# Performance work log

Measured on AMD Instinct MI355X. Metric: run time of the kernel, lower is better.

## Reference

```python
import jax, jax.numpy as jnp
import numpy as np

B, N, C = 4, 1029, 1024
H = 16           # num_heads
L = 8            # num_blocks
DH = C // H      # head_dim = 64
HID = 4 * C      # mlp hidden
SCALE = DH ** -0.5
EPS = 1e-6


def _ln(x, w, b):
    mu = jnp.mean(x, axis=-1, keepdims=True)
    var = jnp.var(x, axis=-1, keepdims=True)
    return (x - mu) * jax.lax.rsqrt(var + EPS) * w + b


def setup_inputs() -> dict:
    key = jax.random.key(0)
    ks = jax.random.split(key, 16)
    s = 0.02
    return {
        "x": jax.random.normal(ks[0], (B, N, C), dtype=jnp.float32),
        "ln1_w": jnp.ones((L, C), jnp.float32),
        "ln1_b": jnp.zeros((L, C), jnp.float32),
        "qkv_w": jax.random.normal(ks[1], (L, 3 * C, C), jnp.float32) * s,
        "qkv_b": jnp.zeros((L, 3 * C), jnp.float32),
        "proj_w": jax.random.normal(ks[2], (L, C, C), jnp.float32) * s,
        "proj_b": jnp.zeros((L, C), jnp.float32),
        "ln2_w": jnp.ones((L, C), jnp.float32),
        "ln2_b": jnp.zeros((L, C), jnp.float32),
        "fc1_w": jax.random.normal(ks[3], (L, HID, C), jnp.float32) * s,
        "fc1_b": jnp.zeros((L, HID), jnp.float32),
        "fc2_w": jax.random.normal(ks[4], (L, C, HID), jnp.float32) * s,
        "fc2_b": jnp.zeros((L, C), jnp.float32),
        "norm_w": jnp.ones((C,), jnp.float32),
        "norm_b": jnp.zeros((C,), jnp.float32),
    }


def _block(x, p):
    ln1_w, ln1_b, qkv_w, qkv_b, proj_w, proj_b, ln2_w, ln2_b, fc1_w, fc1_b, fc2_w, fc2_b = p
    # --- attention (manual fp32 QK^T / softmax / AV, as in Attention.forward) ---
    h = _ln(x, ln1_w, ln1_b)
    qkv = h @ qkv_w.T + qkv_b                        # [B,N,3C]
    qkv = qkv.reshape(B, N, 3, H, DH).transpose(2, 0, 3, 1, 4)  # [3,B,H,N,DH]
    q, k, v = qkv[0], qkv[1], qkv[2]
    attn = jnp.einsum("bhnd,bhmd->bhnm", q.astype(jnp.float32), k.astype(jnp.float32)) * SCALE
    # original subtracts row max before softmax; jax.nn.softmax is the same stable math
    attn = jax.nn.softmax(attn, axis=-1).astype(v.dtype)
    o = jnp.einsum("bhnm,bhmd->bhnd", attn, v)       # [B,H,N,DH]
    o = o.transpose(0, 2, 1, 3).reshape(B, N, C)
    x = x + (o @ proj_w.T + proj_b)
    # --- MLP (exact GELU, as nn.GELU default) ---
    h = _ln(x, ln2_w, ln2_b)
    h = jax.nn.gelu(h @ fc1_w.T + fc1_b, approximate=False)
    x = x + (h @ fc2_w.T + fc2_b)
    return x


def reference(x, ln1_w, ln1_b, qkv_w, qkv_b, proj_w, proj_b, ln2_w, ln2_b,
              fc1_w, fc1_b, fc2_w, fc2_b, norm_w, norm_b):
    params = (ln1_w, ln1_b, qkv_w, qkv_b, proj_w, proj_b, ln2_w, ln2_b,
              fc1_w, fc1_b, fc2_w, fc2_b)

    def body(h, p):
        return _block(h, p), None

    x, _ = jax.lax.scan(body, x, params)
    return _ln(x, norm_w, norm_b)
```

## Files before the change

kernel.cpp:

```cpp
#include <hip/hip_runtime.h>
#include <cstdint>
#include <cstddef>

#define B_    4
#define N_TOK 1029
#define C_    1024
#define H_    16
#define L_    8
#define HID_  4096
#define M_TOK (B_*N_TOK)
#define MP2_  4352
#define TM0_  4096
#define PROWS 4224
#define KVB_  128
#define KVT2_ 9
#define KPAD_ 1152

typedef float f32x4 __attribute__((ext_vector_type(4)));
typedef short bf16x8 __attribute__((ext_vector_type(8)));

__device__ __forceinline__ uint16_t f2bf(float f) {
  uint32_t u = __float_as_uint(f);
  u += 0x7fffu + ((u >> 16) & 1u);
  return (uint16_t)(u >> 16);
}

__device__ __forceinline__ void async_copy16(const uint16_t* src, uint16_t* lds_dst) {
  __builtin_amdgcn_global_load_lds(
      (const __attribute__((address_space(1))) void*)src,
      (__attribute__((address_space(3))) void*)lds_dst, 16, 0, 0);
}

__device__ __forceinline__ int swz16(int row, int byte_in_row) {
  return row * 128 + (byte_in_row ^ ((row & 7) << 4));
}

__global__ __launch_bounds__(256)
void cvt_f32_bf16(const float* __restrict__ in, uint16_t* __restrict__ out, int n4) {
  int i = blockIdx.x * 256 + threadIdx.x;
  if (i < n4) {
    float4 v = reinterpret_cast<const float4*>(in)[i];
    uint64_t pk = (uint64_t)f2bf(v.x) | ((uint64_t)f2bf(v.y) << 16)
                | ((uint64_t)f2bf(v.z) << 32) | ((uint64_t)f2bf(v.w) << 48);
    reinterpret_cast<uint64_t*>(out)[i] = pk;
  }
}

template<int OUTMODE>
__global__ __launch_bounds__(256)
void ln_fwd(const float* __restrict__ x, const float* __restrict__ w,
            const float* __restrict__ b, void* __restrict__ outp) {
  const int row = blockIdx.x;
  const int tid = threadIdx.x;
  const float4 v = reinterpret_cast<const float4*>(x + (size_t)row * C_)[tid];
  float s  = v.x + v.y + v.z + v.w;
  float s2 = v.x*v.x + v.y*v.y + v.z*v.z + v.w*v.w;
  #pragma unroll
  for (int d = 1; d < 64; d <<= 1) {
    s  += __shfl_xor(s, d);
    s2 += __shfl_xor(s2, d);
  }
  __shared__ float red[8];
  const int wv = tid >> 6;
  if ((tid & 63) == 0) { red[wv] = s; red[wv + 4] = s2; }
  __syncthreads();
  s  = red[0] + red[1] + red[2] + red[3];
  s2 = red[4] + red[5] + red[6] + red[7];
  const float mu = s * (1.0f / C_);
  const float rs = rsqrtf(fmaxf(s2 * (1.0f / C_) - mu * mu, 0.0f) + 1e-6f);
  const float4 wv4 = reinterpret_cast<const float4*>(w)[tid];
  const float4 bv4 = reinterpret_cast<const float4*>(b)[tid];
  const float o0 = (v.x - mu) * rs * wv4.x + bv4.x;
  const float o1 = (v.y - mu) * rs * wv4.y + bv4.y;
  const float o2 = (v.z - mu) * rs * wv4.z + bv4.z;
  const float o3 = (v.w - mu) * rs * wv4.w + bv4.w;
  if (OUTMODE == 0) {
    uint64_t pk = (uint64_t)f2bf(o0) | ((uint64_t)f2bf(o1) << 16)
                | ((uint64_t)f2bf(o2) << 32) | ((uint64_t)f2bf(o3) << 48);
    reinterpret_cast<uint64_t*>((uint16_t*)outp + (size_t)row * C_)[tid] = pk;
  } else {
    float4 o; o.x = o0; o.y = o1; o.z = o2; o.w = o3;
    reinterpret_cast<float4*>((float*)outp + (size_t)row * C_)[tid] = o;
  }
}

template<int EPI>
__device__ __forceinline__ void epi_store(int m, int col, float v, int Nn, int kc,
    const float* bias, uint16_t* outb, float* pbuf,
    uint16_t* Qp, uint16_t* Kp, uint16_t* VTp) {
  if (EPI == 3) {
    pbuf[((size_t)kc * PROWS + m) * Nn + col] = v;
  } else if (EPI == 1) {
    const float vb = v + bias[col];
    const float u = -1.5957691216f * (vb + 0.044715f * vb * vb * vb);
    const float g = vb * __builtin_amdgcn_rcpf(1.0f + __expf(u));
    outb[(size_t)m * Nn + col] = f2bf(g);
  } else {
    if (m < M_TOK) {
      const float vb = v + bias[col];
      const int which = col >> 10;
      const int h = (col >> 6) & 15;
      const int d = col & 63;
      const int b = m / N_TOK;
      const int key = m - b * N_TOK;
      const int bh = b * 16 + h;
      if (which == 0)      Qp[((size_t)bh * KPAD_ + key) * 64 + d] = f2bf(vb * 0.125f);
      else if (which == 1) Kp[((size_t)bh * KPAD_ + key) * 64 + d] = f2bf(vb);
      else                 VTp[((size_t)bh * 64 + d) * KPAD_ + key] = f2bf(vb);
    }
  }
}

template<int EPI, int SPLIT>
__global__ __launch_bounds__(512)
void gemm8p(const uint16_t* __restrict__ A, const uint16_t* __restrict__ W,
            const float* __restrict__ bias, uint16_t* __restrict__ outb,
            float* __restrict__ pbuf,
            uint16_t* __restrict__ Qp, uint16_t* __restrict__ Kp,
            uint16_t* __restrict__ VTp, int Nn, int Ktot) {
  const int nbn = Nn >> 8;
  const int MAIN = 16 * nbn * SPLIT;
  const int KC = Ktot / SPLIT;
  const int nwg = (int)gridDim.x;
  const int q8 = nwg >> 3, r8 = nwg & 7;
  const int xcd = (int)blockIdx.x & 7, pos = (int)blockIdx.x >> 3;
  const int wgid = (xcd < r8 ? xcd * (q8 + 1) : r8 * (q8 + 1) + (xcd - r8) * q8) + pos;
  const int tid = (int)threadIdx.x;

  if (wgid >= MAIN) {
    if (tid >= 256) return;
    const int tailid = wgid - MAIN;
    const int tnb = Nn >> 7;
    const int tbn = tailid % tnb, tkc = tailid / tnb;
    const int l = tid & 63, w2 = tid >> 6;
    const int l15 = l & 15, l4 = l >> 4;
    const int wr = w2 >> 1, wc = w2 & 1;
    const uint16_t* Ag = A + (size_t)(TM0_ + wr * 64) * Ktot + (size_t)tkc * KC;
    const uint16_t* Wg = W + (size_t)(tbn * 128 + wc * 64) * Ktot + (size_t)tkc * KC;
    f32x4 acc[4][4] = {};
    const int ks = KC >> 5;
    for (int s = 0; s < ks; ++s) {
      bf16x8 af[4], bf[4];
      #pragma unroll
      for (int i = 0; i < 4; ++i)
        af[i] = *(const bf16x8*)(Ag + (size_t)(i * 16 + l15) * Ktot + s * 32 + l4 * 8);
      #pragma unroll
      for (int j = 0; j < 4; ++j)
        bf[j] = *(const bf16x8*)(Wg + (size_t)(j * 16 + l15) * Ktot + s * 32 + l4 * 8);
      #pragma unroll
      for (int i = 0; i < 4; ++i)
        #pragma unroll
        for (int j = 0; j < 4; ++j)
          acc[i][j] = __builtin_amdgcn_mfma_f32_16x16x32_bf16(af[i], bf[j], acc[i][j], 0, 0, 0);
    }
    #pragma unroll
    for (int j = 0; j < 4; ++j) {
      const int col = tbn * 128 + wc * 64 + j * 16 + l15;
      #pragma unroll
      for (int i = 0; i < 4; ++i) {
        #pragma unroll
        for (int r = 0; r < 4; ++r) {
          const int m = TM0_ + wr * 64 + i * 16 + l4 * 4 + r;
          epi_store<EPI>(m, col, acc[i][j][r], Nn, tkc, bias, outb, pbuf, Qp, Kp, VTp);
        }
      }
    }
    return;
  }

  __shared__ char lds[131072];
  const int kc  = (SPLIT > 1) ? wgid / (16 * nbn) : 0;
  const int rem = (SPLIT > 1) ? wgid % (16 * nbn) : wgid;
  const int bm = rem & 15, bn = rem >> 4;
  const int l = tid & 63, w = tid >> 6;
  const int l15 = l & 15, l4 = l >> 4;
  const int wr = w >> 2, wc = w & 3;

  const uint16_t* Ag = A + (size_t)bm * 256 * Ktot + (size_t)kc * KC;
  const uint16_t* Wg = W + (size_t)bn * 256 * Ktot + (size_t)kc * KC;

  const int srow = tid >> 3;
  const int schunk = (tid & 7) ^ (srow & 7);
  auto stage = [&](int mat, int j, int toff, int pdst) {
    const int rbase = mat ? (j * 64) : ((j & 1) * 128 + ((j >> 1)) * 64);
    const uint16_t* src = (mat ? Wg : Ag)
        + (size_t)(rbase + srow) * Ktot + toff + schunk * 8;
    uint16_t* dst = (uint16_t*)(lds + pdst * 65536 + mat * 32768 + rbase * 128 + tid * 16);
    async_copy16(src, dst);
  };

  const int csel0 = ((l4) ^ (l15 & 7)) * 16;
  const int csel1 = ((4 + l4) ^ (l15 & 7)) * 16;

  f32x4 acc[8][4] = {};
  stage(1, 0, 0, 0); stage(1, 1, 0, 0); stage(1, 2, 0, 0); stage(1, 3, 0, 0);
  stage(0, 0, 0, 0); stage(0, 1, 0, 0); stage(0, 2, 0, 0); stage(0, 3, 0, 0);

  const int nt = KC >> 6;
  bf16x8 bfr[2][4];
  for (int t = 0; t < nt; ++t) {
    const int p = t & 1;
    const char* base = lds + p * 65536;
    const int toff = (t + 1) * 64;
    const bool more = (t + 1 < nt);
    asm volatile("s_waitcnt vmcnt(2)" ::: "memory");
    __builtin_amdgcn_sched_barrier(0);
    __builtin_amdgcn_s_barrier();
    bf16x8 afr[4][2];
    #pragma unroll
    for (int f = 0; f < 4; ++f) {
      const int rb = (wr * 128 + f * 16 + l15) * 128;
      afr[f][0] = *(const bf16x8*)(base + rb + csel0);
      afr[f][1] = *(const bf16x8*)(base + rb + csel1);
    }
    #pragma unroll
    for (int nf = 0; nf < 4; ++nf) {
      const int rb = 32768 + (wc * 64 + nf * 16 + l15) * 128;
      bfr[0][nf] = *(const bf16x8*)(base + rb + csel0);
      bfr[1][nf] = *(const bf16x8*)(base + rb + csel1);
    }
    if (more) {
      stage(1, 0, toff, p ^ 1); stage(1, 1, toff, p ^ 1);
      stage(1, 2, toff, p ^ 1); stage(1, 3, toff, p ^ 1);
      stage(0, 0, toff, p ^ 1); stage(0, 1, toff, p ^ 1);
    }
    __builtin_amdgcn_s_setprio(1);
    #pragma unroll
    for (int kk = 0; kk < 2; ++kk)
      #pragma unroll
      for (int f = 0; f < 4; ++f)
        #pragma unroll
        for (int nf = 0; nf < 4; ++nf)
          acc[f][nf] = __builtin_amdgcn_mfma_f32_16x16x32_bf16(afr[f][kk], bfr[kk][nf], acc[f][nf], 0, 0, 0);
    __builtin_amdgcn_s_setprio(0);
    if (t == nt - 1) asm volatile("s_waitcnt vmcnt(0)" ::: "memory");
    else             asm volatile("s_waitcnt vmcnt(6)" ::: "memory");
    __builtin_amdgcn_sched_barrier(0);
    __builtin_amdgcn_s_barrier();
    #pragma unroll
    for (int f = 0; f < 4; ++f) {
      const int rb = (wr * 128 + 64 + f * 16 + l15) * 128;
      afr[f][0] = *(const bf16x8*)(base + rb + csel0);
      afr[f][1] = *(const bf16x8*)(base + rb + csel1);
    }
    if (more) { stage(0, 2, toff, p ^ 1); stage(0, 3, toff, p ^ 1); }
    __builtin_amdgcn_s_setprio(1);
    #pragma unroll
    for (int kk = 0; kk < 2; ++kk)
      #pragma unroll
      for (int f = 0; f < 4; ++f)
        #pragma unroll
        for (int nf = 0; nf < 4; ++nf)
          acc[4 + f][nf] = __builtin_amdgcn_mfma_f32_16x16x32_bf16(afr[f][kk], bfr[kk][nf], acc[4 + f][nf], 0, 0, 0);
    __builtin_amdgcn_s_setprio(0);
  }

  #pragma unroll
  for (int nf = 0; nf < 4; ++nf) {
    const int col = bn * 256 + wc * 64 + nf * 16 + l15;
    #pragma unroll
    for (int mf = 0; mf < 8; ++mf) {
      const int mb = bm * 256 + wr * 128 + mf * 16 + l4 * 4;
      #pragma unroll
      for (int r = 0; r < 4; ++r)
        epi_store<EPI>(mb + r, col, acc[mf][nf][r], Nn, kc, bias, outb, pbuf, Qp, Kp, VTp);
    }
  }
}

template<int KCH>
__global__ __launch_bounds__(256)
void reduce_add(const float* __restrict__ pbuf, const float* __restrict__ bias,
                float* __restrict__ xbuf) {
  const int m = blockIdx.x;
  const int c4 = threadIdx.x;
  float4 s = reinterpret_cast<const float4*>(bias)[c4];
  #pragma unroll
  for (int kc = 0; kc < KCH; ++kc) {
    const float4 pv = reinterpret_cast<const float4*>(pbuf + ((size_t)kc * PROWS + m) * C_)[c4];
    s.x += pv.x; s.y += pv.y; s.z += pv.z; s.w += pv.w;
  }
  float4 x = reinterpret_cast<float4*>(xbuf + (size_t)m * C_)[c4];
  x.x += s.x; x.y += s.y; x.z += s.z; x.w += s.w;
  reinterpret_cast<float4*>(xbuf + (size_t)m * C_)[c4] = x;
}

__global__ __launch_bounds__(256, 3)
void attn_fwd(const uint16_t* __restrict__ Qp, const uint16_t* __restrict__ Kp,
              const uint16_t* __restrict__ VTp, uint16_t* __restrict__ ob) {
  __shared__ uint16_t Ksm_[KVB_ * 64];
  __shared__ uint16_t Vsm_[64 * KVB_];
  __shared__ uint16_t Psm_[4][16 * 136];

  const int tid = (int)threadIdx.x;
  const int l = tid & 63, w = tid >> 6;
  const int l15 = l & 15, l4 = l >> 4;
  const int bh = (int)blockIdx.x;
  const int qt = (int)blockIdx.y;

  const uint16_t* Kb = Kp + (size_t)bh * KPAD_ * 64;
  const uint16_t* Vb = VTp + (size_t)bh * 64 * KPAD_;

  bf16x8 qf[2];
  {
    const int qrow = qt * 64 + w * 16 + l15;
    const uint16_t* qbase = Qp + ((size_t)bh * KPAD_ + qrow) * 64;
    qf[0] = *(const bf16x8*)(qbase + l4 * 8);
    qf[1] = *(const bf16x8*)(qbase + 32 + l4 * 8);
  }

  float mrow = -1e30f, lrow = 0.0f;
  f32x4 oacc[4] = {};

  const int krow_s = tid >> 3;
  const int kslot_s = (tid & 7) ^ (krow_s & 7);
  const int vd_s = tid >> 4;
  const int vslot_s = (tid & 15) ^ (vd_s & 15);

  for (int kt = 0; kt < KVT2_; ++kt) {
    const int key0 = kt * KVB_;
    __syncthreads();
    #pragma unroll
    for (int it = 0; it < 4; ++it) {
      const int row = it * 32 + krow_s;
      async_copy16(Kb + (size_t)(key0 + row) * 64 + kslot_s * 8,
                   Ksm_ + it * 2048 + tid * 8);
    }
    #pragma unroll
    for (int it = 0; it < 4; ++it) {
      const int d = it * 16 + vd_s;
      async_copy16(Vb + (size_t)d * KPAD_ + key0 + vslot_s * 8,
                   Vsm_ + it * 2048 + tid * 8);
    }
    __syncthreads();

    f32x4 s[8];
    #pragma unroll
    for (int kf = 0; kf < 8; ++kf) s[kf] = f32x4{0.f, 0.f, 0.f, 0.f};
    #pragma unroll
    for (int kk = 0; kk < 2; ++kk) {
      #pragma unroll
      for (int kf = 0; kf < 8; ++kf) {
        const bf16x8 kfrag = *(const bf16x8*)((const char*)Ksm_ + swz16(kf * 16 + l15, kk * 64 + l4 * 16));
        s[kf] = __builtin_amdgcn_mfma_f32_16x16x32_bf16(kfrag, qf[kk], s[kf], 0, 0, 0);
      }
    }
    if (kt == KVT2_ - 1) {
      #pragma unroll
      for (int kf = 0; kf < 8; ++kf)
        #pragma unroll
        for (int r = 0; r < 4; ++r)
          if (key0 + kf * 16 + l4 * 4 + r >= N_TOK) s[kf][r] = -1e30f;
    }
    float pmx = s[0][0];
    #pragma unroll
    for (int kf = 0; kf < 8; ++kf)
      #pragma unroll
      for (int r = 0; r < 4; ++r) pmx = fmaxf(pmx, s[kf][r]);
    pmx = fmaxf(pmx, __shfl_xor(pmx, 16));
    pmx = fmaxf(pmx, __shfl_xor(pmx, 32));
    if (!__all(pmx - mrow <= 8.0f)) {
      const float mi = fmaxf(mrow, pmx);
      const float sc = __expf(mrow - mi);
      mrow = mi;
      lrow *= sc;
      #pragma unroll
      for (int df = 0; df < 4; ++df)
        #pragma unroll
        for (int r = 0; r < 4; ++r) oacc[df][r] *= sc;
    }
    float psum = 0.0f;
    #pragma unroll
    for (int kf = 0; kf < 8; ++kf) {
      const float p0 = __expf(s[kf][0] - mrow);
      const float p1 = __expf(s[kf][1] - mrow);
      const float p2 = __expf(s[kf][2] - mrow);
      const float p3 = __expf(s[kf][3] - mrow);
      psum += (p0 + p1) + (p2 + p3);
      const uint64_t pk = (uint64_t)f2bf(p0) | ((uint64_t)f2bf(p1) << 16)
                        | ((uint64_t)f2bf(p2) << 32) | ((uint64_t)f2bf(p3) << 48);
      *(uint64_t*)(&Psm_[w][l15 * 136 + kf * 16 + l4 * 4]) = pk;
    }
    psum += __shfl_xor(psum, 16);
    psum += __shfl_xor(psum, 32);
    lrow += psum;
    #pragma unroll
    for (int kk = 0; kk < 4; ++kk) {
      const bf16x8 pf = *(const bf16x8*)(&Psm_[w][l15 * 136 + kk * 32 + l4 * 8]);
      #pragma unroll
      for (int df = 0; df < 4; ++df) {
        const int d = df * 16 + l15;
        const bf16x8 vfrag = *(const bf16x8*)(Vsm_ + d * KVB_ + (((kk * 4 + l4) ^ (d & 15)) * 8));
        oacc[df] = __builtin_amdgcn_mfma_f32_16x16x32_bf16(vfrag, pf, oacc[df], 0, 0, 0);
      }
    }
  }

  const int q = qt * 64 + w * 16 + l15;
  if (q < N_TOK) {
    const float inv = 1.0f / lrow;
    const int m = (bh >> 4) * N_TOK + q;
    const int hbase = (bh & 15) * 64;
    #pragma unroll
    for (int df = 0; df < 4; ++df)
      #pragma unroll
      for (int r = 0; r < 4; ++r) {
        const int c = hbase + df * 16 + l4 * 4 + r;
        ob[(size_t)m * C_ + c] = f2bf(oacc[df][r] * inv);
      }
  }
}

extern "C" void kernel_launch(void* const* d_in, const int* in_sizes, int n_in,
                              void* d_out, int out_size, void* d_ws, size_t ws_size,
                              hipStream_t stream) {
  const float* x_in   = (const float*)d_in[0];
  const float* ln1_w  = (const float*)d_in[1];
  const float* ln1_b  = (const float*)d_in[2];
  const float* qkv_w  = (const float*)d_in[3];
  const float* qkv_b  = (const float*)d_in[4];
  const float* proj_w = (const float*)d_in[5];
  const float* proj_b = (const float*)d_in[6];
  const float* ln2_w  = (const float*)d_in[7];
  const float* ln2_b  = (const float*)d_in[8];
  const float* fc1_w  = (const float*)d_in[9];
  const float* fc1_b  = (const float*)d_in[10];
  const float* fc2_w  = (const float*)d_in[11];
  const float* fc2_b  = (const float*)d_in[12];
  const float* norm_w = (const float*)d_in[13];
  const float* norm_b = (const float*)d_in[14];

  char* p = (char*)d_ws;
  float*    xbuf = (float*)p;     p += (size_t)MP2_ * C_ * 4;
  uint16_t* hbuf = (uint16_t*)p;  p += (size_t)MP2_ * C_ * 2;
  uint16_t* big  = (uint16_t*)p;  p += (size_t)MP2_ * HID_ * 2;
  uint16_t* wq   = (uint16_t*)p;  p += (size_t)L_ * 3 * C_ * C_ * 2;
  uint16_t* wp   = (uint16_t*)p;  p += (size_t)L_ * C_ * C_ * 2;
  uint16_t* w1   = (uint16_t*)p;  p += (size_t)L_ * HID_ * C_ * 2;
  uint16_t* w2   = (uint16_t*)p;  p += (size_t)L_ * C_ * HID_ * 2;
  uint16_t* qp   = (uint16_t*)p;  p += (size_t)64 * KPAD_ * 64 * 2;
  uint16_t* kp   = (uint16_t*)p;  p += (size_t)64 * KPAD_ * 64 * 2;
  uint16_t* vtp  = (uint16_t*)p;  p += (size_t)64 * 64 * KPAD_ * 2;
  float*    pbuf = (float*)p;     p += (size_t)4 * PROWS * C_ * 4;
  if ((size_t)(p - (char*)d_ws) > ws_size) return;

  hipMemcpyAsync(xbuf, x_in, (size_t)M_TOK * C_ * sizeof(float),
                 hipMemcpyDeviceToDevice, stream);

  auto cvt = [&](const float* src, uint16_t* dst, size_t n) {
    const int n4 = (int)(n / 4);
    cvt_f32_bf16<<<dim3((n4 + 255) / 256), dim3(256), 0, stream>>>(src, dst, n4);
  };
  cvt(qkv_w,  wq, (size_t)L_ * 3 * C_ * C_);
  cvt(proj_w, wp, (size_t)L_ * C_ * C_);
  cvt(fc1_w,  w1, (size_t)L_ * HID_ * C_);
  cvt(fc2_w,  w2, (size_t)L_ * C_ * HID_);

  for (int lyr = 0; lyr < L_; ++lyr) {
    ln_fwd<0><<<dim3(M_TOK), dim3(256), 0, stream>>>(
        xbuf, ln1_w + (size_t)lyr * C_, ln1_b + (size_t)lyr * C_, hbuf);
    gemm8p<0, 1><<<dim3(216), dim3(512), 0, stream>>>(
        hbuf, wq + (size_t)lyr * 3 * C_ * C_, qkv_b + (size_t)lyr * 3 * C_,
        nullptr, nullptr, qp, kp, vtp, 3 * C_, C_);
    attn_fwd<<<dim3(64, 17), dim3(256), 0, stream>>>(qp, kp, vtp, hbuf);
    gemm8p<3, 2><<<dim3(144), dim3(512), 0, stream>>>(
        hbuf, wp + (size_t)lyr * C_ * C_, nullptr,
        nullptr, pbuf, nullptr, nullptr, nullptr, C_, C_);
    reduce_add<2><<<dim3(M_TOK), dim3(256), 0, stream>>>(
        pbuf, proj_b + (size_t)lyr * C_, xbuf);
    ln_fwd<0><<<dim3(M_TOK), dim3(256), 0, stream>>>(
        xbuf, ln2_w + (size_t)lyr * C_, ln2_b + (size_t)lyr * C_, hbuf);
    gemm8p<1, 1><<<dim3(288), dim3(512), 0, stream>>>(
        hbuf, w1 + (size_t)lyr * HID_ * C_, fc1_b + (size_t)lyr * HID_,
        big, nullptr, nullptr, nullptr, nullptr, HID_, C_);
    gemm8p<3, 4><<<dim3(288), dim3(512), 0, stream>>>(
        big, w2 + (size_t)lyr * C_ * HID_, nullptr,
        nullptr, pbuf, nullptr, nullptr, nullptr, C_, HID_);
    reduce_add<4><<<dim3(M_TOK), dim3(256), 0, stream>>>(
        pbuf, fc2_b + (size_t)lyr * C_, xbuf);
  }
  ln_fwd<1><<<dim3(M_TOK), dim3(256), 0, stream>>>(xbuf, norm_w, norm_b, d_out);
}
```

Measured before the change: 2.770 ms.

## Fuse split-K reduction with LayerNorm and add 128-row GEMM for proj/MLP

Adds a reduce_ln kernel that sums the split-K partials, applies the residual add and computes the following LayerNorm in one pass. This drops the separate ln_fwd launches and one extra read/write of the residual stream per sub-block. It also adds a simpler gemm_s kernel with 128x256 tiles covering all 33 row blocks and no tail path, used for proj (now split-K 4), fc1 and fc2. The new GEMM does single-buffered LDS staging with no pipelining, which may lower per-tile efficiency in exchange for better CU fill.

```diff
diff --git a/kernel.cpp b/kernel.cpp
--- a/kernel.cpp
+++ b/kernel.cpp
@@ -74,13 +74,55 @@
   const float o1 = (v.y - mu) * rs * wv4.y + bv4.y;
   const float o2 = (v.z - mu) * rs * wv4.z + bv4.z;
   const float o3 = (v.w - mu) * rs * wv4.w + bv4.w;
-  if (OUTMODE == 0) {
+  uint64_t pk = (uint64_t)f2bf(o0) | ((uint64_t)f2bf(o1) << 16)
+              | ((uint64_t)f2bf(o2) << 32) | ((uint64_t)f2bf(o3) << 48);
+  reinterpret_cast<uint64_t*>((uint16_t*)outp + (size_t)row * C_)[tid] = pk;
+}
+
+template<int KCH, int OUT>
+__global__ __launch_bounds__(256)
+void reduce_ln(const float* __restrict__ pbuf, const float* __restrict__ bias,
+               float* __restrict__ xbuf, const float* __restrict__ lw,
+               const float* __restrict__ lb, void* __restrict__ outp) {
+  const int m = blockIdx.x;
+  const int c4 = threadIdx.x;
+  float4 s = reinterpret_cast<const float4*>(bias)[c4];
+  #pragma unroll
+  for (int kc = 0; kc < KCH; ++kc) {
+    const float4 pv = reinterpret_cast<const float4*>(pbuf + ((size_t)kc * PROWS + m) * C_)[c4];
+    s.x += pv.x; s.y += pv.y; s.z += pv.z; s.w += pv.w;
+  }
+  float4 x = reinterpret_cast<float4*>(xbuf + (size_t)m * C_)[c4];
+  x.x += s.x; x.y += s.y; x.z += s.z; x.w += s.w;
+  reinterpret_cast<float4*>(xbuf + (size_t)m * C_)[c4] = x;
+  float ss  = x.x + x.y + x.z + x.w;
+  float ss2 = x.x*x.x + x.y*x.y + x.z*x.z + x.w*x.w;
+  #pragma unroll
+  for (int d = 1; d < 64; d <<= 1) {
+    ss  += __shfl_xor(ss, d);
+    ss2 += __shfl_xor(ss2, d);
+  }
+  __shared__ float red[8];
+  const int wv = c4 >> 6;
+  if ((c4 & 63) == 0) { red[wv] = ss; red[wv + 4] = ss2; }
+  __syncthreads();
+  ss  = red[0] + red[1] + red[2] + red[3];
+  ss2 = red[4] + red[5] + red[6] + red[7];
+  const float mu = ss * (1.0f / C_);
+  const float rs = rsqrtf(fmaxf(ss2 * (1.0f / C_) - mu * mu, 0.0f) + 1e-6f);
+  const float4 wv4 = reinterpret_cast<const float4*>(lw)[c4];
+  const float4 bv4 = reinterpret_cast<const float4*>(lb)[c4];
+  const float o0 = (x.x - mu) * rs * wv4.x + bv4.x;
+  const float o1 = (x.y - mu) * rs * wv4.y + bv4.y;
+  const float o2 = (x.z - mu) * rs * wv4.z + bv4.z;
+  const float o3 = (x.w - mu) * rs * wv4.w + bv4.w;
+  if (OUT == 0) {
     uint64_t pk = (uint64_t)f2bf(o0) | ((uint64_t)f2bf(o1) << 16)
                 | ((uint64_t)f2bf(o2) << 32) | ((uint64_t)f2bf(o3) << 48);
-    reinterpret_cast<uint64_t*>((uint16_t*)outp + (size_t)row * C_)[tid] = pk;
+    reinterpret_cast<uint64_t*>((uint16_t*)outp + (size_t)m * C_)[c4] = pk;
   } else {
     float4 o; o.x = o0; o.y = o1; o.z = o2; o.w = o3;
-    reinterpret_cast<float4*>((float*)outp + (size_t)row * C_)[tid] = o;
+    reinterpret_cast<float4*>((float*)outp + (size_t)m * C_)[c4] = o;
   }
 }
 
@@ -89,7 +131,7 @@
     const float* bias, uint16_t* outb, float* pbuf,
     uint16_t* Qp, uint16_t* Kp, uint16_t* VTp) {
   if (EPI == 3) {
-    pbuf[((size_t)kc * PROWS + m) * Nn + col] = v;
+    pbuf[((size_t)kc * PROWS + m) * C_ + col] = v;
   } else if (EPI == 1) {
     const float vb = v + bias[col];
     const float u = -1.5957691216f * (vb + 0.044715f * vb * vb * vb);
@@ -112,6 +154,86 @@
 }
 
 template<int EPI, int SPLIT>
+__global__ __launch_bounds__(512, 4)
+void gemm_s(const uint16_t* __restrict__ A, const uint16_t* __restrict__ W,
+            const float* __restrict__ bias, uint16_t* __restrict__ outb,
+            float* __restrict__ pbuf, int Nn, int Ktot) {
+  const int nbn = Nn >> 8;
+  const int KC = Ktot / SPLIT;
+  const int nwg = (int)gridDim.x;
+  const int q8 = nwg >> 3, r8 = nwg & 7;
+  const int xcd = (int)blockIdx.x & 7, pos = (int)blockIdx.x >> 3;
+  const int wgid = (xcd < r8 ? xcd * (q8 + 1) : r8 * (q8 + 1) + (xcd - r8) * q8) + pos;
+  const int kc  = wgid / (33 * nbn);
+  const int rem = wgid % (33 * nbn);
+  const int bm = rem % 33, bn = rem / 33;
+
+  const int tid = (int)threadIdx.x;
+  const int l = tid & 63, w = tid >> 6;
+  const int l15 = l & 15, l4 = l >> 4;
+  const int wr = w >> 2, wc = w & 3;
+
+  __shared__ char lds[49152];
+
+  const uint16_t* Ag = A + (size_t)bm * 128 * Ktot + (size_t)kc * KC;
+  const uint16_t* Wg = W + (size_t)bn * 256 * Ktot + (size_t)kc * KC;
+
+  const int srow = tid >> 3;
+  const int schunk = (tid & 7) ^ (srow & 7);
+  const int csel0 = ((l4) ^ (l15 & 7)) << 4;
+  const int csel1 = ((4 + l4) ^ (l15 & 7)) << 4;
+
+  f32x4 acc[4][4] = {};
+  const int nt = KC >> 6;
+  for (int t = 0; t < nt; ++t) {
+    const int toff = t * 64;
+    __syncthreads();
+    #pragma unroll
+    for (int j = 0; j < 2; ++j) {
+      const int row = j * 64 + srow;
+      async_copy16(Ag + (size_t)row * Ktot + toff + schunk * 8,
+                   (uint16_t*)(lds + j * 8192 + tid * 16));
+    }
+    #pragma unroll
+    for (int j = 0; j < 4; ++j) {
+      const int row = j * 64 + srow;
+      async_copy16(Wg + (size_t)row * Ktot + toff + schunk * 8,
+                   (uint16_t*)(lds + 16384 + j * 8192 + tid * 16));
+    }
+    __syncthreads();
+    #pragma unroll
+    for (int kk = 0; kk < 2; ++kk) {
+      const int cs = kk ? csel1 : csel0;
+      bf16x8 afr[4], bfr[4];
+      #pragma unroll
+      for (int f = 0; f < 4; ++f)
+        afr[f] = *(const bf16x8*)(lds + (wr * 64 + f * 16 + l15) * 128 + cs);
+      #pragma unroll
+      for (int nf = 0; nf < 4; ++nf)
+        bfr[nf] = *(const bf16x8*)(lds + 16384 + (wc * 64 + nf * 16 + l15) * 128 + cs);
+      #pragma unroll
+      for (int f = 0; f < 4; ++f)
+        #pragma unroll
+        for (int nf = 0; nf < 4; ++nf)
+          acc[f][nf] = __builtin_amdgcn_mfma_f32_16x16x32_bf16(afr[f], bfr[nf], acc[f][nf], 0, 0, 0);
+    }
+  }
+
+  #pragma unroll
+  for (int nf = 0; nf < 4; ++nf) {
+    const int col = bn * 256 + wc * 64 + nf * 16 + l15;
+    #pragma unroll
+    for (int mf = 0; mf < 4; ++mf) {
+      const int mb = bm * 128 + wr * 64 + mf * 16 + l4 * 4;
+      #pragma unroll
+      for (int r = 0; r < 4; ++r)
+        epi_store<EPI>(mb + r, col, acc[mf][nf][r], Nn, kc, bias, outb, pbuf,
+                       nullptr, nullptr, nullptr);
+    }
+  }
+}
+
+template<int EPI, int SPLIT>
 __global__ __launch_bounds__(512)
 void gemm8p(const uint16_t* __restrict__ A, const uint16_t* __restrict__ W,
             const float* __restrict__ bias, uint16_t* __restrict__ outb,
@@ -157,13 +279,12 @@
     for (int j = 0; j < 4; ++j) {
       const int col = tbn * 128 + wc * 64 + j * 16 + l15;
       #pragma unroll
-      for (int i = 0; i < 4; ++i) {
+      for (int i = 0; i < 4; ++i)
         #pragma unroll
         for (int r = 0; r < 4; ++r) {
           const int m = TM0_ + wr * 64 + i * 16 + l4 * 4 + r;
           epi_store<EPI>(m, col, acc[i][j][r], Nn, tkc, bias, outb, pbuf, Qp, Kp, VTp);
         }
-      }
     }
     return;
   }
@@ -266,23 +387,6 @@
         epi_store<EPI>(mb + r, col, acc[mf][nf][r], Nn, kc, bias, outb, pbuf, Qp, Kp, VTp);
     }
   }
-}
-
-template<int KCH>
-__global__ __launch_bounds__(256)
-void reduce_add(const float* __restrict__ pbuf, const float* __restrict__ bias,
-                float* __restrict__ xbuf) {
-  const int m = blockIdx.x;
-  const int c4 = threadIdx.x;
-  float4 s = reinterpret_cast<const float4*>(bias)[c4];
-  #pragma unroll
-  for (int kc = 0; kc < KCH; ++kc) {
-    const float4 pv = reinterpret_cast<const float4*>(pbuf + ((size_t)kc * PROWS + m) * C_)[c4];
-    s.x += pv.x; s.y += pv.y; s.z += pv.z; s.w += pv.w;
-  }
-  float4 x = reinterpret_cast<float4*>(xbuf + (size_t)m * C_)[c4];
-  x.x += s.x; x.y += s.y; x.z += s.z; x.w += s.w;
-  reinterpret_cast<float4*>(xbuf + (size_t)m * C_)[c4] = x;
 }
 
 __global__ __launch_bounds__(256, 3)
@@ -456,28 +560,30 @@
   cvt(fc1_w,  w1, (size_t)L_ * HID_ * C_);
   cvt(fc2_w,  w2, (size_t)L_ * C_ * HID_);
 
+  ln_fwd<0><<<dim3(M_TOK), dim3(256), 0, stream>>>(xbuf, ln1_w, ln1_b, hbuf);
+
   for (int lyr = 0; lyr < L_; ++lyr) {
-    ln_fwd<0><<<dim3(M_TOK), dim3(256), 0, stream>>>(
-        xbuf, ln1_w + (size_t)lyr * C_, ln1_b + (size_t)lyr * C_, hbuf);
     gemm8p<0, 1><<<dim3(216), dim3(512), 0, stream>>>(
         hbuf, wq + (size_t)lyr * 3 * C_ * C_, qkv_b + (size_t)lyr * 3 * C_,
         nullptr, nullptr, qp, kp, vtp, 3 * C_, C_);
     attn_fwd<<<dim3(64, 17), dim3(256), 0, stream>>>(qp, kp, vtp, hbuf);
-    gemm8p<3, 2><<<dim3(144), dim3(512), 0, stream>>>(
-        hbuf, wp + (size_t)lyr * C_ * C_, nullptr,
-        nullptr, pbuf, nullptr, nullptr, nullptr, C_, C_);
-    reduce_add<2><<<dim3(M_TOK), dim3(256), 0, stream>>>(
-        pbuf, proj_b + (size_t)lyr * C_, xbuf);
-    ln_fwd<0><<<dim3(M_TOK), dim3(256), 0, stream>>>(
-        xbuf, ln2_w + (size_t)lyr * C_, ln2_b + (size_t)lyr * C_, hbuf);
-    gemm8p<1, 1><<<dim3(288), dim3(512), 0, stream>>>(
+    gemm_s<3, 4><<<dim3(528), dim3(512), 0, stream>>>(
+        hbuf, wp + (size_t)lyr * C_ * C_, nullptr, nullptr, pbuf, C_, C_);
+    reduce_ln<4, 0><<<dim3(M_TOK), dim3(256), 0, stream>>>(
+        pbuf, proj_b + (size_t)lyr * C_, xbuf,
+        ln2_w + (size_t)lyr * C_, ln2_b + (size_t)lyr * C_, hbuf);
+    gemm_s<1, 1><<<dim3(528), dim3(512), 0, stream>>>(
         hbuf, w1 + (size_t)lyr * HID_ * C_, fc1_b + (size_t)lyr * HID_,
-        big, nullptr, nullptr, nullptr, nullptr, HID_, C_);
-    gemm8p<3, 4><<<dim3(288), dim3(512), 0, stream>>>(
-        big, w2 + (size_t)lyr * C_ * HID_, nullptr,
-        nullptr, pbuf, nullptr, nullptr, nullptr, C_, HID_);
-    reduce_add<4><<<dim3(M_TOK), dim3(256), 0, stream>>>(
-        pbuf, fc2_b + (size_t)lyr * C_, xbuf);
-  }
-  ln_fwd<1><<<dim3(M_TOK), dim3(256), 0, stream>>>(xbuf, norm_w, norm_b, d_out);
-}
+        big, nullptr, HID_, C_);
+    gemm_s<3, 4><<<dim3(528), dim3(512), 0, stream>>>(
+        big, w2 + (size_t)lyr * C_ * HID_, nullptr, nullptr, pbuf, C_, HID_);
+    if (lyr < L_ - 1) {
+      reduce_ln<4, 0><<<dim3(M_TOK), dim3(256), 0, stream>>>(
+          pbuf, fc2_b + (size_t)lyr * C_, xbuf,
+          ln1_w + (size_t)(lyr + 1) * C_, ln1_b + (size_t)(lyr + 1) * C_, hbuf);
+    } else {
+      reduce_ln<4, 1><<<dim3(M_TOK), dim3(256), 0, stream>>>(
+          pbuf, fc2_b + (size_t)lyr * C_, xbuf, norm_w, norm_b, d_out);
+    }
+  }
+}
```

New measurement: 2.675 ms. 1.04x faster.
